# Optimization experiments

Measured on AMD Instinct MI355X. Metric: run time of the kernel, lower is better.

The kernel has to match this reference:

```python
import jax, jax.numpy as jnp
import numpy as np

N_WIRES = 14
LATENT_DIM = 8
N_OPS = 50

# ---- fixed random-layer circuit structure (mirrors tq.RandomLayer) ----
_rng = np.random.default_rng(1234)
_types = _rng.integers(0, 4, size=N_OPS)  # 0:RX 1:RY 2:RZ 3:CRX
_wires = []
for _t in _types:
    if _t < 3:
        _wires.append((int(_rng.integers(0, N_WIRES)), -1))
    else:
        _w = _rng.choice(N_WIRES, size=2, replace=False)
        _wires.append((int(_w[0]), int(_w[1])))
GATE_SPEC = list(zip(_types.tolist(), _wires))

# PauliZ eigenvalue signs per wire, per basis state: [n_wires, 2^n]
_idx = np.arange(2 ** N_WIRES)
Z_SIGNS = jnp.asarray(
    np.stack([1.0 - 2.0 * ((_idx >> (N_WIRES - 1 - i)) & 1) for i in range(N_WIRES)]),
    dtype=jnp.float32)


def _rx(theta):
    c = jnp.cos(theta / 2).astype(jnp.complex64)
    s = jnp.sin(theta / 2).astype(jnp.complex64)
    return jnp.stack([jnp.stack([c, -1j * s], -1),
                      jnp.stack([-1j * s, c], -1)], -2)


def _ry(theta):
    c = jnp.cos(theta / 2).astype(jnp.complex64)
    s = jnp.sin(theta / 2).astype(jnp.complex64)
    return jnp.stack([jnp.stack([c, -s], -1),
                      jnp.stack([s, c], -1)], -2)


def _rz(theta):
    e = jnp.exp(-0.5j * theta.astype(jnp.complex64))
    z = jnp.zeros_like(e)
    return jnp.stack([jnp.stack([e, z], -1),
                      jnp.stack([z, jnp.conj(e)], -1)], -2)


def _crx(theta):
    m = jnp.eye(4, dtype=jnp.complex64)
    return m.at[2:, 2:].set(_rx(theta))


def _apply_1q(state, gate, w):
    # state: [bsz] + [2]*N_WIRES ; gate: [2,2] or [bsz,2,2]
    bsz = state.shape[0]
    st = jnp.moveaxis(state, w + 1, 1).reshape(bsz, 2, -1)
    if gate.ndim == 2:
        st = jnp.einsum('ab,kbr->kar', gate, st)
    else:
        st = jnp.einsum('kab,kbr->kar', gate, st)
    st = st.reshape((bsz, 2) + (2,) * (N_WIRES - 1))
    return jnp.moveaxis(st, 1, w + 1)


def _apply_2q(state, gate, w0, w1):
    bsz = state.shape[0]
    st = jnp.moveaxis(state, (w0 + 1, w1 + 1), (1, 2)).reshape(bsz, 4, -1)
    st = jnp.einsum('ab,kbr->kar', gate, st)
    st = st.reshape((bsz, 2, 2) + (2,) * (N_WIRES - 2))
    return jnp.moveaxis(st, (1, 2), (w0 + 1, w1 + 1))


def setup_inputs() -> dict:
    key = jax.random.key(0)
    k1, k2 = jax.random.split(key)
    x = jax.random.normal(k1, (256, N_WIRES), dtype=jnp.float32)
    rl_params = jax.random.normal(k2, (N_OPS,), dtype=jnp.float32)
    return {"x": x, "rl_params": rl_params}


def reference(x, rl_params):
    bsz = x.shape[0]
    # |0...0> initial state
    state = jnp.zeros((bsz,) + (2,) * N_WIRES, dtype=jnp.complex64)
    state = state.at[(slice(None),) + (0,) * N_WIRES].set(1.0)
    # angle encoding: RX(x[:, i]) on wire i (batched gate)
    for i in range(N_WIRES):
        state = _apply_1q(state, _rx(x[:, i]), i)
    # random layer: 50 fixed-structure gates with trainable angles
    for k, (t, (w0, w1)) in enumerate(GATE_SPEC):
        p = rl_params[k]
        if t == 0:
            state = _apply_1q(state, _rx(p), w0)
        elif t == 1:
            state = _apply_1q(state, _ry(p), w0)
        elif t == 2:
            state = _apply_1q(state, _rz(p), w0)
        else:
            state = _apply_2q(state, _crx(p), w0, w1)
    probs = jnp.abs(state.reshape(bsz, -1)) ** 2          # [bsz, 2^n]
    expz = probs @ Z_SIGNS.T                               # [bsz, n_wires]
    return expz[:, :LATENT_DIM]
```

## Files before the change

### kernel.cpp

```cpp
#include <hip/hip_runtime.h>
#include <cstdint>

#define N_WIRES 14
#define N_OPS   50
#define NSTATE  (1 << N_WIRES)
#define BSZ     256
#define BLOCK   1024
#define LATENT  8
#define NCLMAX  50

namespace cg {
typedef unsigned __int128 u128;
struct PCG { u128 state; u128 inc; bool has32; uint32_t buf32; };

constexpr u128 pcg_mult() {
  return (((u128)2549297995355413924ULL) << 64) | 4865540595714422341ULL;
}
constexpr uint64_t n64(PCG &s) {
  s.state = s.state * pcg_mult() + s.inc;
  uint64_t x = (uint64_t)(s.state >> 64) ^ (uint64_t)s.state;
  unsigned r = (unsigned)(s.state >> 122);
  return (x >> (r & 63)) | (x << ((64 - r) & 63));
}
constexpr uint32_t n32(PCG &s) {
  if (s.has32) { s.has32 = false; return s.buf32; }
  uint64_t n = n64(s);
  s.has32 = true; s.buf32 = (uint32_t)(n >> 32);
  return (uint32_t)n;
}
constexpr uint32_t hashmix(uint32_t v, uint32_t &hc) {
  v ^= hc; hc *= 0x931e8875u; v *= hc; v ^= v >> 16; return v;
}
constexpr uint32_t mixf(uint32_t x, uint32_t y) {
  uint32_t r = x * 0xca01f9ddu - y * 0x4973f715u;
  r ^= r >> 16; return r;
}
constexpr PCG seedseq(uint32_t entropy) {
  uint32_t pool[4] = {0, 0, 0, 0};
  uint32_t hc = 0x43b0d7e5u;
  pool[0] = hashmix(entropy, hc);
  for (int i = 1; i < 4; i++) pool[i] = hashmix(0u, hc);
  for (int s = 0; s < 4; s++)
    for (int d = 0; d < 4; d++)
      if (s != d) pool[d] = mixf(pool[d], hashmix(pool[s], hc));
  uint32_t w[8] = {};
  uint32_t hb = 0x8b51f9ddu;
  for (int i = 0; i < 8; i++) {
    uint32_t dv = pool[i & 3];
    dv ^= hb; hb *= 0x58f38dedu; dv *= hb; dv ^= dv >> 16; w[i] = dv;
  }
  uint64_t v0 = (uint64_t)w[0] | ((uint64_t)w[1] << 32);
  uint64_t v1 = (uint64_t)w[2] | ((uint64_t)w[3] << 32);
  uint64_t v2 = (uint64_t)w[4] | ((uint64_t)w[5] << 32);
  uint64_t v3 = (uint64_t)w[6] | ((uint64_t)w[7] << 32);
  PCG r{};
  u128 initstate = ((u128)v0 << 64) | v1;
  u128 initseq   = ((u128)v2 << 64) | v3;
  r.inc = (initseq << 1) | 1;
  r.state = 0;
  r.state = r.state * pcg_mult() + r.inc;
  r.state += initstate;
  r.state = r.state * pcg_mult() + r.inc;
  r.has32 = false; r.buf32 = 0;
  return r;
}
constexpr uint32_t lem32(PCG &r, uint32_t rmax) {
  uint32_t ex = rmax + 1u;
  uint64_t m = (uint64_t)n32(r) * ex;
  uint32_t lo = (uint32_t)m;
  if (lo < ex) {
    uint32_t t = (0xFFFFFFFFu - rmax) % ex;
    while (lo < t) { m = (uint64_t)n32(r) * ex; lo = (uint32_t)m; }
  }
  return (uint32_t)(m >> 32);
}

struct SchedC {
  int ncl;
  int cpos[NCLMAX * 3];
  int cng[NCLMAX];
  int cgoff[NCLMAX];
  int gpk[N_OPS];
};

constexpr SchedC make_sched() {
  int gt[N_OPS] = {}, g0[N_OPS] = {}, g1[N_OPS] = {};
  {
    PCG r = seedseq(1234u);
    for (int i = 0; i < N_OPS; i++) gt[i] = (int)lem32(r, 3);
    for (int i = 0; i < N_OPS; i++) {
      if (gt[i] < 3) { g0[i] = (int)lem32(r, 13); g1[i] = -1; continue; }
      uint32_t a = lem32(r, 12);
      uint32_t v = lem32(r, 13);
      uint32_t b = (v == a) ? 13u : v;
      uint32_t j = lem32(r, 1);
      if (j == 0) { uint32_t t = a; a = b; b = t; }
      g0[i] = (int)a; g1[i] = (int)b;
    }
  }
  SchedC S{};
  bool done[N_OPS] = {};
  int nsched = 0, ncl = 0, gcount = 0;
  while (nsched < N_OPS) {
    int posv[3] = {}, posn = 0;
    int clg[N_OPS] = {}, ncg = 0;
    bool progress = true;
    while (progress) {
      progress = false;
      for (int i = 0; i < N_OPS; i++) {
        if (done[i]) continue;
        bool avail = true;
        for (int j = 0; j < i && avail; j++) {
          if (done[j]) continue;
          if (g0[j] == g0[i] || (g1[i] >= 0 && g0[j] == g1[i])) avail = false;
          else if (g1[j] >= 0 && (g1[j] == g0[i] || (g1[i] >= 0 && g1[j] == g1[i]))) avail = false;
        }
        if (!avail) continue;
        int p0 = 13 - g0[i];
        int p1 = (g1[i] >= 0) ? (13 - g1[i]) : -1;
        bool h0 = false, h1 = (p1 < 0);
        for (int k = 0; k < posn; k++) {
          if (posv[k] == p0) h0 = true;
          if (p1 >= 0 && posv[k] == p1) h1 = true;
        }
        int need = (h0 ? 0 : 1) + ((p1 >= 0 && !h1) ? 1 : 0);
        if (posn + need > 3) continue;
        if (!h0) posv[posn++] = p0;
        if (p1 >= 0 && !h1) posv[posn++] = p1;
        clg[ncg++] = i;
        done[i] = true; nsched++; progress = true;
      }
    }
    for (int p = 0; posn < 3 && p < 14; p++) {
      bool used = false;
      for (int k = 0; k < posn; k++) if (posv[k] == p) used = true;
      if (!used) posv[posn++] = p;
    }
    for (int a = 0; a < 2; a++)
      for (int b2 = a + 1; b2 < 3; b2++)
        if (posv[b2] < posv[a]) { int t = posv[a]; posv[a] = posv[b2]; posv[b2] = t; }
    for (int k = 0; k < 3; k++) S.cpos[ncl * 3 + k] = posv[k];
    S.cng[ncl] = ncg;
    S.cgoff[ncl] = gcount;
    for (int e = 0; e < ncg; e++) {
      int i = clg[e];
      int pa = 13 - g0[i], la = 0;
      for (int k = 0; k < 3; k++) if (posv[k] == pa) la = k;
      int lt = 0;
      if (g1[i] >= 0) {
        int pt = 13 - g1[i];
        for (int k = 0; k < 3; k++) if (posv[k] == pt) lt = k;
      }
      S.gpk[gcount++] = gt[i] | (la << 2) | (lt << 4) | (i << 6);
    }
    ncl++;
  }
  S.ncl = ncl;
  return S;
}

constexpr SchedC SC = make_sched();

constexpr int swzc(int i) { return i ^ (((i >> 4) ^ (i >> 8) ^ (i >> 12)) & 15); }
}

__device__ __forceinline__ int swzd(int i) {
  return i ^ (((i >> 4) ^ (i >> 8) ^ (i >> 12)) & 15);
}

#define RXP(I0, I1) { float r0 = Ar[I0], q0_ = Ai[I0], r1 = Ar[I1], q1_ = Ai[I1]; \
  Ar[I0] = cc * r0 + ss * q1_; Ai[I0] = cc * q0_ - ss * r1; \
  Ar[I1] = cc * r1 + ss * q0_; Ai[I1] = cc * q1_ - ss * r0; }
#define RYP(I0, I1) { float r0 = Ar[I0], q0_ = Ai[I0], r1 = Ar[I1], q1_ = Ai[I1]; \
  Ar[I0] = cc * r0 - ss * r1; Ai[I0] = cc * q0_ - ss * q1_; \
  Ar[I1] = ss * r0 + cc * r1; Ai[I1] = ss * q0_ + cc * q1_; }
#define RZP(I0, I1) { float r0 = Ar[I0], q0_ = Ai[I0], r1 = Ar[I1], q1_ = Ai[I1]; \
  Ar[I0] = cc * r0 + ss * q0_; Ai[I0] = cc * q0_ - ss * r0; \
  Ar[I1] = cc * r1 - ss * q1_; Ai[I1] = cc * q1_ + ss * r1; }

template<int PK>
__device__ __forceinline__ void one_gate(float Ar[8], float Ai[8], const float2 *coef) {
  constexpr int t = PK & 3, la = (PK >> 2) & 3, lt = (PK >> 4) & 3, gi = PK >> 6;
  const float2 cs = coef[gi];
  const float cc = cs.x, ss = cs.y;
  if constexpr (t == 0) {
    if constexpr (la == 0)      { RXP(0,1) RXP(2,3) RXP(4,5) RXP(6,7) }
    else if constexpr (la == 1) { RXP(0,2) RXP(1,3) RXP(4,6) RXP(5,7) }
    else                        { RXP(0,4) RXP(1,5) RXP(2,6) RXP(3,7) }
  } else if constexpr (t == 1) {
    if constexpr (la == 0)      { RYP(0,1) RYP(2,3) RYP(4,5) RYP(6,7) }
    else if constexpr (la == 1) { RYP(0,2) RYP(1,3) RYP(4,6) RYP(5,7) }
    else                        { RYP(0,4) RYP(1,5) RYP(2,6) RYP(3,7) }
  } else if constexpr (t == 2) {
    if constexpr (la == 0)      { RZP(0,1) RZP(2,3) RZP(4,5) RZP(6,7) }
    else if constexpr (la == 1) { RZP(0,2) RZP(1,3) RZP(4,6) RZP(5,7) }
    else                        { RZP(0,4) RZP(1,5) RZP(2,6) RZP(3,7) }
  } else {
    constexpr int cse = la * 3 + lt;
    if constexpr (cse == 1)      { RXP(1,3) RXP(5,7) }
    else if constexpr (cse == 2) { RXP(1,5) RXP(3,7) }
    else if constexpr (cse == 3) { RXP(2,3) RXP(6,7) }
    else if constexpr (cse == 5) { RXP(2,6) RXP(3,7) }
    else if constexpr (cse == 6) { RXP(4,5) RXP(6,7) }
    else                         { RXP(4,6) RXP(5,7) }
  }
}

template<int GOFF, int NG, int E>
__device__ __forceinline__ void gates_rec(float Ar[8], float Ai[8], const float2 *coef) {
  if constexpr (E < NG) {
    one_gate<cg::SC.gpk[GOFF + E]>(Ar, Ai, coef);
    gates_rec<GOFF, NG, E + 1>(Ar, Ai, coef);
  }
}

template<int C>
__device__ __forceinline__ void do_cluster(float2 *st, const float2 *coef, int tid,
                                           float (&pr)[LATENT]) {
  constexpr int q0 = cg::SC.cpos[3 * C], q1 = cg::SC.cpos[3 * C + 1], q2 = cg::SC.cpos[3 * C + 2];
  constexpr int ng = cg::SC.cng[C], goff = cg::SC.cgoff[C];
  constexpr int m0 = 1 << q0, m1 = 1 << q1, m2 = 1 << q2;
  constexpr bool LAST = (C == cg::SC.ncl - 1);
  constexpr int s1 = cg::swzc(m0),           s2 = cg::swzc(m1);
  constexpr int s3 = cg::swzc(m0 | m1),      s4 = cg::swzc(m2);
  constexpr int s5 = cg::swzc(m0 | m2),      s6 = cg::swzc(m1 | m2);
  constexpr int s7 = cg::swzc(m0 | m1 | m2);

  #pragma unroll 1
  for (int grp = 0; grp < 2; ++grp) {
    int bi = tid + (grp << 10);
    bi = ((bi >> q0) << (q0 + 1)) | (bi & (m0 - 1));
    bi = ((bi >> q1) << (q1 + 1)) | (bi & (m1 - 1));
    bi = ((bi >> q2) << (q2 + 1)) | (bi & (m2 - 1));
    const int sb = swzd(bi);

    float Ar[8], Ai[8];
    { float2 v = st[sb];      Ar[0] = v.x; Ai[0] = v.y; }
    { float2 v = st[sb ^ s1]; Ar[1] = v.x; Ai[1] = v.y; }
    { float2 v = st[sb ^ s2]; Ar[2] = v.x; Ai[2] = v.y; }
    { float2 v = st[sb ^ s3]; Ar[3] = v.x; Ai[3] = v.y; }
    { float2 v = st[sb ^ s4]; Ar[4] = v.x; Ai[4] = v.y; }
    { float2 v = st[sb ^ s5]; Ar[5] = v.x; Ai[5] = v.y; }
    { float2 v = st[sb ^ s6]; Ar[6] = v.x; Ai[6] = v.y; }
    { float2 v = st[sb ^ s7]; Ar[7] = v.x; Ai[7] = v.y; }

    gates_rec<goff, ng, 0>(Ar, Ai, coef);

    if constexpr (!LAST) {
      st[sb]      = make_float2(Ar[0], Ai[0]);
      st[sb ^ s1] = make_float2(Ar[1], Ai[1]);
      st[sb ^ s2] = make_float2(Ar[2], Ai[2]);
      st[sb ^ s3] = make_float2(Ar[3], Ai[3]);
      st[sb ^ s4] = make_float2(Ar[4], Ai[4]);
      st[sb ^ s5] = make_float2(Ar[5], Ai[5]);
      st[sb ^ s6] = make_float2(Ar[6], Ai[6]);
      st[sb ^ s7] = make_float2(Ar[7], Ai[7]);
    } else {
      #pragma unroll
      for (int j = 0; j < 8; j++) {
        float p2 = Ar[j] * Ar[j] + Ai[j] * Ai[j];
        int idx = bi | ((j & 1) ? m0 : 0) | ((j & 2) ? m1 : 0) | ((j & 4) ? m2 : 0);
        #pragma unroll
        for (int w = 0; w < LATENT; w++)
          pr[w] += ((idx >> (13 - w)) & 1) ? -p2 : p2;
      }
    }
  }
  if constexpr (!LAST) __syncthreads();
}

template<int C>
__device__ __forceinline__ void clusters_rec(float2 *st, const float2 *coef, int tid,
                                             float (&pr)[LATENT]) {
  if constexpr (C < cg::SC.ncl) {
    do_cluster<C>(st, coef, tid, pr);
    clusters_rec<C + 1>(st, coef, tid, pr);
  }
}

__global__ __launch_bounds__(BLOCK) void qae_k(
    const float* __restrict__ x, const float* __restrict__ rlp,
    float* __restrict__ out)
{
  __shared__ float2 st[NSTATE];
  __shared__ float encc[N_WIRES], encs[N_WIRES];
  __shared__ float2 coef[N_OPS];
  const int b = blockIdx.x, tid = threadIdx.x;

  if (tid < N_WIRES) {
    float a = 0.5f * x[b * N_WIRES + tid];
    encc[tid] = cosf(a); encs[tid] = sinf(a);
  } else if (tid >= 64 && tid < 64 + N_OPS) {
    int g = tid - 64;
    float a = 0.5f * rlp[g];
    coef[g] = make_float2(cosf(a), sinf(a));
  }
  __syncthreads();

  #pragma unroll 1
  for (int k = tid; k < NSTATE; k += BLOCK) {
    float r = 1.0f;
    #pragma unroll
    for (int p = 0; p < N_WIRES; p++)
      r *= ((k >> p) & 1) ? encs[13 - p] : encc[13 - p];
    int pc = __popc((unsigned)k) & 3;
    st[swzd(k)] = make_float2((pc == 0) ? r : ((pc == 2) ? -r : 0.0f),
                              (pc == 1) ? -r : ((pc == 3) ? r : 0.0f));
  }
  __syncthreads();

  float pr[LATENT];
  #pragma unroll
  for (int w = 0; w < LATENT; w++) pr[w] = 0.0f;

  clusters_rec<0>(st, coef, tid, pr);

  #pragma unroll
  for (int w = 0; w < LATENT; w++) {
    float v = pr[w];
    #pragma unroll
    for (int off = 32; off >= 1; off >>= 1) v += __shfl_down(v, off, 64);
    pr[w] = v;
  }
  __syncthreads();
  float* red = (float*)st;
  const int wave = tid >> 6, lane = tid & 63;
  if (lane == 0) {
    #pragma unroll
    for (int w = 0; w < LATENT; w++) red[wave * LATENT + w] = pr[w];
  }
  __syncthreads();
  if (tid < LATENT) {
    float v = 0.0f;
    #pragma unroll
    for (int wv = 0; wv < BLOCK / 64; wv++) v += red[wv * LATENT + tid];
    out[b * LATENT + tid] = v;
  }
}

extern "C" void kernel_launch(void* const* d_in, const int* in_sizes, int n_in,
                              void* d_out, int out_size, void* d_ws, size_t ws_size,
                              hipStream_t stream) {
  const float *x   = (const float*)d_in[0];
  const float *rlp = (const float*)d_in[1];
  float *out = (float*)d_out;

  qae_k<<<dim3(BSZ), dim3(BLOCK), 0, stream>>>(x, rlp, out);
}
```

Before: 42.52 us.

## Treat diagonal RZ and CRX control wires as non-local to shrink cluster count

The gate scheduler now reserves one of the three register-resident qubit positions only for wires that need an amplitude swap: RX/RY targets and CRX targets. RZ gates and CRX controls on wires outside the cluster are applied using the thread's base index bit, as a per-thread phase or as a conditional rotation. This lets more gates fit into each 3-qubit cluster, cutting the number of shared-memory load/store passes over the state vector. In exchange, each gate does a little per-thread select arithmetic, and the packed gate encoding changes layout.

```diff
diff --git a/kernel.cpp b/kernel.cpp
--- a/kernel.cpp
+++ b/kernel.cpp
@@ -116,17 +116,17 @@
           else if (g1[j] >= 0 && (g1[j] == g0[i] || (g1[i] >= 0 && g1[j] == g1[i]))) avail = false;
         }
         if (!avail) continue;
-        int p0 = 13 - g0[i];
-        int p1 = (g1[i] >= 0) ? (13 - g1[i]) : -1;
-        bool h0 = false, h1 = (p1 < 0);
-        for (int k = 0; k < posn; k++) {
-          if (posv[k] == p0) h0 = true;
-          if (p1 >= 0 && posv[k] == p1) h1 = true;
+        int sw = -1;
+        if (gt[i] == 0 || gt[i] == 1) sw = 13 - g0[i];
+        else if (gt[i] == 3) sw = 13 - g1[i];
+        int need = 0;
+        if (sw >= 0) {
+          bool h = false;
+          for (int k = 0; k < posn; k++) if (posv[k] == sw) h = true;
+          if (!h) need = 1;
         }
-        int need = (h0 ? 0 : 1) + ((p1 >= 0 && !h1) ? 1 : 0);
         if (posn + need > 3) continue;
-        if (!h0) posv[posn++] = p0;
-        if (p1 >= 0 && !h1) posv[posn++] = p1;
+        if (need) posv[posn++] = sw;
         clg[ncg++] = i;
         done[i] = true; nsched++; progress = true;
       }
@@ -143,15 +143,23 @@
     S.cng[ncl] = ncg;
     S.cgoff[ncl] = gcount;
     for (int e = 0; e < ncg; e++) {
-      int i = clg[e];
-      int pa = 13 - g0[i], la = 0;
-      for (int k = 0; k < 3; k++) if (posv[k] == pa) la = k;
-      int lt = 0;
-      if (g1[i] >= 0) {
+      int i = clg[e], t = gt[i];
+      int A = 0, mode = 0, lt = 0;
+      if (t <= 1) {
+        int p = 13 - g0[i];
+        for (int k = 0; k < 3; k++) if (posv[k] == p) A = k;
+      } else if (t == 2) {
+        int p = 13 - g0[i], s = -1;
+        for (int k = 0; k < 3; k++) if (posv[k] == p) s = k;
+        if (s >= 0) { A = s; mode = 0; } else { A = p; mode = 1; }
+      } else {
         int pt = 13 - g1[i];
         for (int k = 0; k < 3; k++) if (posv[k] == pt) lt = k;
-      }
-      S.gpk[gcount++] = gt[i] | (la << 2) | (lt << 4) | (i << 6);
+        int p = 13 - g0[i], s = -1;
+        for (int k = 0; k < 3; k++) if (posv[k] == p) s = k;
+        if (s >= 0) { A = s; mode = 0; } else { A = p; mode = 1; }
+      }
+      S.gpk[gcount++] = t | (A << 2) | (mode << 6) | (lt << 7) | (i << 9);
     }
     ncl++;
   }
@@ -179,38 +187,61 @@
   Ar[I1] = cc * r1 - ss * q1_; Ai[I1] = cc * q1_ + ss * r1; }
 
 template<int PK>
-__device__ __forceinline__ void one_gate(float Ar[8], float Ai[8], const float2 *coef) {
-  constexpr int t = PK & 3, la = (PK >> 2) & 3, lt = (PK >> 4) & 3, gi = PK >> 6;
+__device__ __forceinline__ void one_gate(float Ar[8], float Ai[8], const float2 *coef, int bi) {
+  constexpr int t = PK & 3, A = (PK >> 2) & 15, mode = (PK >> 6) & 1,
+                lt = (PK >> 7) & 3, gi = PK >> 9;
   const float2 cs = coef[gi];
   const float cc = cs.x, ss = cs.y;
   if constexpr (t == 0) {
-    if constexpr (la == 0)      { RXP(0,1) RXP(2,3) RXP(4,5) RXP(6,7) }
-    else if constexpr (la == 1) { RXP(0,2) RXP(1,3) RXP(4,6) RXP(5,7) }
-    else                        { RXP(0,4) RXP(1,5) RXP(2,6) RXP(3,7) }
+    if constexpr (A == 0)      { RXP(0,1) RXP(2,3) RXP(4,5) RXP(6,7) }
+    else if constexpr (A == 1) { RXP(0,2) RXP(1,3) RXP(4,6) RXP(5,7) }
+    else                       { RXP(0,4) RXP(1,5) RXP(2,6) RXP(3,7) }
   } else if constexpr (t == 1) {
-    if constexpr (la == 0)      { RYP(0,1) RYP(2,3) RYP(4,5) RYP(6,7) }
-    else if constexpr (la == 1) { RYP(0,2) RYP(1,3) RYP(4,6) RYP(5,7) }
-    else                        { RYP(0,4) RYP(1,5) RYP(2,6) RYP(3,7) }
+    if constexpr (A == 0)      { RYP(0,1) RYP(2,3) RYP(4,5) RYP(6,7) }
+    else if constexpr (A == 1) { RYP(0,2) RYP(1,3) RYP(4,6) RYP(5,7) }
+    else                       { RYP(0,4) RYP(1,5) RYP(2,6) RYP(3,7) }
   } else if constexpr (t == 2) {
-    if constexpr (la == 0)      { RZP(0,1) RZP(2,3) RZP(4,5) RZP(6,7) }
-    else if constexpr (la == 1) { RZP(0,2) RZP(1,3) RZP(4,6) RZP(5,7) }
-    else                        { RZP(0,4) RZP(1,5) RZP(2,6) RZP(3,7) }
+    if constexpr (mode == 0) {
+      if constexpr (A == 0)      { RZP(0,1) RZP(2,3) RZP(4,5) RZP(6,7) }
+      else if constexpr (A == 1) { RZP(0,2) RZP(1,3) RZP(4,6) RZP(5,7) }
+      else                       { RZP(0,4) RZP(1,5) RZP(2,6) RZP(3,7) }
+    } else {
+      const float sb_ = ((bi >> A) & 1) ? ss : -ss;
+      #pragma unroll
+      for (int j = 0; j < 8; j++) {
+        float r0 = Ar[j], q0_ = Ai[j];
+        Ar[j] = cc * r0 - sb_ * q0_;
+        Ai[j] = cc * q0_ + sb_ * r0;
+      }
+    }
   } else {
-    constexpr int cse = la * 3 + lt;
-    if constexpr (cse == 1)      { RXP(1,3) RXP(5,7) }
-    else if constexpr (cse == 2) { RXP(1,5) RXP(3,7) }
-    else if constexpr (cse == 3) { RXP(2,3) RXP(6,7) }
-    else if constexpr (cse == 5) { RXP(2,6) RXP(3,7) }
-    else if constexpr (cse == 6) { RXP(4,5) RXP(6,7) }
-    else                         { RXP(4,6) RXP(5,7) }
+    if constexpr (mode == 0) {
+      constexpr int cse = A * 3 + lt;
+      if constexpr (cse == 1)      { RXP(1,3) RXP(5,7) }
+      else if constexpr (cse == 2) { RXP(1,5) RXP(3,7) }
+      else if constexpr (cse == 3) { RXP(2,3) RXP(6,7) }
+      else if constexpr (cse == 5) { RXP(2,6) RXP(3,7) }
+      else if constexpr (cse == 6) { RXP(4,5) RXP(6,7) }
+      else                         { RXP(4,6) RXP(5,7) }
+    } else {
+      const int bc = (bi >> A) & 1;
+      const float cce = bc ? cc : 1.0f;
+      const float sse = bc ? ss : 0.0f;
+      {
+        const float cc = cce, ss = sse;
+        if constexpr (lt == 0)      { RXP(0,1) RXP(2,3) RXP(4,5) RXP(6,7) }
+        else if constexpr (lt == 1) { RXP(0,2) RXP(1,3) RXP(4,6) RXP(5,7) }
+        else                        { RXP(0,4) RXP(1,5) RXP(2,6) RXP(3,7) }
+      }
+    }
   }
 }
 
 template<int GOFF, int NG, int E>
-__device__ __forceinline__ void gates_rec(float Ar[8], float Ai[8], const float2 *coef) {
+__device__ __forceinline__ void gates_rec(float Ar[8], float Ai[8], const float2 *coef, int bi) {
   if constexpr (E < NG) {
-    one_gate<cg::SC.gpk[GOFF + E]>(Ar, Ai, coef);
-    gates_rec<GOFF, NG, E + 1>(Ar, Ai, coef);
+    one_gate<cg::SC.gpk[GOFF + E]>(Ar, Ai, coef, bi);
+    gates_rec<GOFF, NG, E + 1>(Ar, Ai, coef, bi);
   }
 }
 
@@ -244,7 +275,7 @@
     { float2 v = st[sb ^ s6]; Ar[6] = v.x; Ai[6] = v.y; }
     { float2 v = st[sb ^ s7]; Ar[7] = v.x; Ai[7] = v.y; }
 
-    gates_rec<goff, ng, 0>(Ar, Ai, coef);
+    gates_rec<goff, ng, 0>(Ar, Ai, coef, bi);
 
     if constexpr (!LAST) {
       st[sb]      = make_float2(Ar[0], Ai[0]);
```

Measured after the change: 76.64 us. 80.2% more time.
